# Performance work log

Hardware: AMD Instinct MI355X
Metric: run time of the kernel (lower is better)

The kernel has to match this reference:

```python
import jax, jax.numpy as jnp
import numpy as np
from jax import lax

N, P = 64, 7
C1, H1 = 256, 56
C2, H2 = 512, 28
C3, H3 = 1024, 14
HID1, HID2, HID3 = 256, 768, 1792
MLP1, MLP2, OUT = 3584, 1792, 512


def setup_inputs() -> dict:
    key = jax.random.key(0)
    ks = jax.random.split(key, 32)
    x1 = jax.random.normal(ks[0], (N, C1, H1, H1), jnp.float32)
    x2 = jax.random.normal(ks[1], (N, C2, H2, H2), jnp.float32)
    x3 = jax.random.normal(ks[2], (N, C3, H3, H3), jnp.float32)
    a = jax.random.randint(ks[3], (N, P, 2), 0, 56)
    b = jax.random.randint(ks[4], (N, P, 2), 0, 56)
    lo, hi = jnp.minimum(a, b), jnp.maximum(a, b)
    patchs = jnp.stack([lo[..., 0], hi[..., 0], lo[..., 1], hi[..., 1]], axis=-1)
    drop = jax.random.bernoulli(ks[5], 0.1, (N, P))
    patchs = jnp.where(drop[..., None], 0, patchs).astype(jnp.int32)

    def lin(k, o, i):
        return jax.random.normal(k, (o, i), jnp.float32) * 0.02

    def vec(k, o):
        return jax.random.normal(k, (o,), jnp.float32) * 0.02

    inp = {
        'x1': x1, 'x2': x2, 'x3': x3, 'patchs': patchs,
        # LSTM weights, torch gate order (i,f,g,o); bias = b_ih + b_hh combined
        'l1_wih': lin(ks[6], 4 * HID1, 256),  'l1_whh': lin(ks[7], 4 * HID1, HID1),  'l1_b': vec(ks[8], 4 * HID1),
        'l2_wih': lin(ks[9], 4 * HID2, 768),  'l2_whh': lin(ks[10], 4 * HID2, HID2), 'l2_b': vec(ks[11], 4 * HID2),
        'l3_wih': lin(ks[12], 4 * HID3, 1792),'l3_whh': lin(ks[13], 4 * HID3, HID3), 'l3_b': vec(ks[14], 4 * HID3),
        'aw1': lin(ks[15], MLP1, P * HID3), 'ab1': vec(ks[16], MLP1),
        'aw2': lin(ks[17], MLP2, MLP1),     'ab2': vec(ks[18], MLP2),
        'aw3': lin(ks[19], P, MLP2),        'ab3': vec(ks[20], P),
        'fw':  lin(ks[21], OUT, HID3),      'fb':  vec(ks[22], OUT),
    }
    return inp


def _crop_avg(x, patchs, num, den):
    """Batched data-dependent crop + avg-pool via 2D integral image.
    x: [N,C,H,W]; patchs: [N,P,4] ints (y0,y1,x0,x1) at 56-scale. Returns [N,P,C]."""
    y0 = (patchs[..., 0] * num) // den
    y1 = (patchs[..., 1] * num) // den
    x0 = (patchs[..., 2] * num) // den
    x1 = (patchs[..., 3] * num) // den
    S = jnp.cumsum(jnp.cumsum(x, axis=2), axis=3)
    S = jnp.pad(S, ((0, 0), (0, 0), (1, 0), (1, 0)))  # [N,C,H+1,W+1]
    bidx = jnp.arange(x.shape[0])[:, None]

    def g(Y, X):
        return S[bidx, :, Y, X]  # advanced idx split by ':' -> [N,P,C]

    tot = g(y1 + 1, x1 + 1) - g(y0, x1 + 1) - g(y1 + 1, x0) + g(y0, x0)
    area = ((y1 - y0 + 1) * (x1 - x0 + 1)).astype(x.dtype)[..., None]
    avg = tot / area
    zero = jnp.all(patchs == 0, axis=-1)  # all-zero box -> zero feature
    return jnp.where(zero[..., None], jnp.zeros((), x.dtype), avg)


def _lstm(x, wih, whh, b):
    """Single-layer batch-first LSTM, torch gate order i,f,g,o. x: [N,T,D] -> [N,T,H]."""
    Nb, T, _ = x.shape
    H = whh.shape[1]
    xg = jnp.einsum('ntd,gd->ntg', x, wih) + b  # precompute input gates

    def step(carry, xt):
        h, c = carry
        gates = xt + h @ whh.T
        i, f, g, o = jnp.split(gates, 4, axis=-1)
        c = jax.nn.sigmoid(f) * c + jax.nn.sigmoid(i) * jnp.tanh(g)
        h = jax.nn.sigmoid(o) * jnp.tanh(c)
        return (h, c), h

    h0 = jnp.zeros((Nb, H), x.dtype)
    _, hs = lax.scan(step, (h0, h0), jnp.swapaxes(xg, 0, 1))
    return jnp.swapaxes(hs, 0, 1)


def reference(x1, x2, x3, patchs,
              l1_wih, l1_whh, l1_b, l2_wih, l2_whh, l2_b, l3_wih, l3_whh, l3_b,
              aw1, ab1, aw2, ab2, aw3, ab3, fw, fb):
    local1 = _crop_avg(x1, patchs, 55, 55)                     # [N,7,256]
    rnn1 = _lstm(local1, l1_wih, l1_whh, l1_b)                 # [N,7,256]
    local2 = jnp.concatenate([_crop_avg(x2, patchs, 27, 55), rnn1], axis=2)   # [N,7,768]
    rnn2 = _lstm(local2, l2_wih, l2_whh, l2_b)                 # [N,7,768]
    local3 = jnp.concatenate([_crop_avg(x3, patchs, 13, 55), rnn2], axis=2)   # [N,7,1792]
    rnn3 = _lstm(local3, l3_wih, l3_whh, l3_b)                 # [N,7,1792]
    # attention pooling (dropout = identity in eval)
    flat = rnn3.reshape(rnn3.shape[0], -1)                     # [N,7*1792]
    h = jax.nn.relu(flat @ aw1.T + ab1)
    h = jax.nn.relu(h @ aw2.T + ab2)
    attn = jax.nn.relu(h @ aw3.T + ab3)                        # [N,7]
    alpha = jax.nn.softmax(attn, axis=1)
    feat = jnp.sum(rnn3 * alpha[:, :, None], axis=1)           # [N,1792]
    return feat @ fw.T + fb                                    # [N,512]
```

## Files before the change

kernel.cpp:

```cpp
#include <hip/hip_runtime.h>
#include <hip/hip_bf16.h>
#include <math.h>

#define NB 64
#define PP 7

typedef __attribute__((ext_vector_type(8))) short short8;
typedef __attribute__((ext_vector_type(4))) float f32x4;

static __device__ inline unsigned bf16r(float f) {
    unsigned u = __builtin_bit_cast(unsigned, f);
    u += 0x7fffu + ((u >> 16) & 1u);
    return u >> 16;
}
static __device__ inline unsigned pack2(float a, float b) {
    return bf16r(a) | (bf16r(b) << 16);
}

template<int H, int VEC, int GRP>
__device__ inline void crop_dev(
    int bx, int n, const float* __restrict__ x, const int* __restrict__ patchs,
    float* __restrict__ out, int C, int num, int den, int ldo, int col0)
{
    constexpr int USED = H / VEC;
    constexpr int PPWAVE = 64 / GRP;
    int tid = threadIdx.x, lane = tid & 63, wv = tid >> 6;
    int sub = lane / GRP, xl = lane & (GRP - 1);
    bool act = xl < USED;
    int c = bx * (4 * PPWAVE) + wv * PPWAVE + sub;

    int y0m1[PP], y1s[PP], x0s[PP], x1s[PP], zer[PP];
    float rarea[PP];
    #pragma unroll
    for (int p = 0; p < PP; ++p) {
        int p0 = patchs[(n * PP + p) * 4 + 0];
        int p1 = patchs[(n * PP + p) * 4 + 1];
        int p2 = patchs[(n * PP + p) * 4 + 2];
        int p3 = patchs[(n * PP + p) * 4 + 3];
        int y0 = p0 * num / den, y1 = p1 * num / den;
        int xx0 = p2 * num / den, xx1 = p3 * num / den;
        y0m1[p] = y0 - 1; y1s[p] = y1; x0s[p] = xx0; x1s[p] = xx1;
        rarea[p] = 1.f / (float)((y1 - y0 + 1) * (xx1 - xx0 + 1));
        zer[p] = (p0 | p1 | p2 | p3) == 0;
    }

    const float* pl = x + ((size_t)n * C + c) * (H * H) + (act ? xl * VEC : 0);

    float cc[VEC];
    float lo[PP][VEC], hi[PP][VEC];
    #pragma unroll
    for (int e = 0; e < VEC; ++e) cc[e] = 0.f;
    #pragma unroll
    for (int p = 0; p < PP; ++p)
        #pragma unroll
        for (int e = 0; e < VEC; ++e) { lo[p][e] = 0.f; hi[p][e] = 0.f; }

    #pragma unroll 4
    for (int y = 0; y < H; ++y) {
        float v[VEC];
        if constexpr (VEC == 4) {
            float4 t = *reinterpret_cast<const float4*>(pl + y * H);
            v[0] = t.x; v[1] = t.y; v[2] = t.z; v[3] = t.w;
        } else {
            float2 t = *reinterpret_cast<const float2*>(pl + y * H);
            v[0] = t.x; v[1] = t.y;
        }
        #pragma unroll
        for (int e = 0; e < VEC; ++e) cc[e] += v[e];
        #pragma unroll
        for (int p = 0; p < PP; ++p) {
            #pragma unroll
            for (int e = 0; e < VEC; ++e) {
                lo[p][e] = (y == y0m1[p]) ? cc[e] : lo[p][e];
                hi[p][e] = (y == y1s[p]) ? cc[e] : hi[p][e];
            }
        }
    }

    #pragma unroll
    for (int p = 0; p < PP; ++p) {
        float d = 0.f;
        #pragma unroll
        for (int e = 0; e < VEC; ++e) {
            int col = xl * VEC + e;
            if (col >= x0s[p] && col <= x1s[p]) d += hi[p][e] - lo[p][e];
        }
        #pragma unroll
        for (int off = GRP / 2; off >= 1; off >>= 1)
            d += __shfl_xor(d, off, 64);
        if (act && xl == 0)
            out[(size_t)(n * PP + p) * ldo + col0 + c] = zer[p] ? 0.f : d * rarea[p];
    }
}

__device__ inline void cvt_dev(
    int b, const float* __restrict__ in, uint4* __restrict__ out, int n8)
{
    int idx = b * 256 + threadIdx.x;
    if (idx >= n8) return;
    const float4* p = reinterpret_cast<const float4*>(in) + 2 * (size_t)idx;
    float4 a = p[0], bb = p[1];
    uint4 v;
    v.x = pack2(a.x, a.y); v.y = pack2(a.z, a.w);
    v.z = pack2(bb.x, bb.y); v.w = pack2(bb.z, bb.w);
    out[idx] = v;
}

__global__ __launch_bounds__(256) void prep_kernel(
    const float* __restrict__ x1, const float* __restrict__ x2,
    const float* __restrict__ x3, const int* __restrict__ patchs,
    float* __restrict__ local1, float* __restrict__ local2,
    float* __restrict__ local3,
    const float* __restrict__ l1_whh, uint4* __restrict__ whh1b,
    const float* __restrict__ l2_whh, uint4* __restrict__ whh2b,
    const float* __restrict__ l3_whh, uint4* __restrict__ whh3b,
    const float* __restrict__ l3_wih, uint4* __restrict__ wih3b)
{
    int b = blockIdx.x;
    if (b < 1024) {
        crop_dev<56, 4, 16>(b & 15, b >> 4, x1, patchs, local1, 256, 55, 55, 256, 0);
    } else if (b < 2048) {
        int bb = b - 1024;
        crop_dev<28, 4, 8>(bb & 15, bb >> 4, x2, patchs, local2, 512, 27, 55, 768, 0);
    } else if (b < 4096) {
        int bb = b - 2048;
        crop_dev<14, 2, 8>(bb & 31, bb >> 5, x3, patchs, local3, 1024, 13, 55, 1792, 0);
    } else if (b < 4224) {
        cvt_dev(b - 4096, l1_whh, whh1b, 32768);
    } else if (b < 5376) {
        cvt_dev(b - 4224, l2_whh, whh2b, 294912);
    } else if (b < 11648) {
        cvt_dev(b - 5376, l3_whh, whh3b, 1605632);
    } else {
        cvt_dev(b - 11648, l3_wih, wih3b, 1605632);
    }
}

template<int BN, bool WBF>
__global__ __launch_bounds__(256) void gemm_kernel(
    const float* __restrict__ X, int ldx,
    const void* __restrict__ Wp, int K,
    const float* __restrict__ bias,
    float* __restrict__ out, int ldo,
    int kchunk, int partial)
{
    constexpr int NF = BN / 64;
    __shared__ short Xs[64][72];
    __shared__ short Ws[BN][72];
    int tid = threadIdx.x;
    int lane = tid & 63, wv = tid >> 6;
    int m0 = blockIdx.y * 64;
    int o0 = blockIdx.x * BN;
    int z = blockIdx.z;
    int kbeg = z * kchunk, kend = kbeg + kchunk;

    f32x4 acc[4][NF];
    #pragma unroll
    for (int i = 0; i < 4; ++i)
        #pragma unroll
        for (int j = 0; j < NF; ++j)
            acc[i][j] = (f32x4){0.f, 0.f, 0.f, 0.f};

    for (int kb = kbeg; kb < kend; kb += 64) {
        #pragma unroll
        for (int i = 0; i < 2; ++i) {
            int cch = tid + 256 * i;
            int r = cch >> 3, col = (cch & 7) * 8;
            const float* src = X + (size_t)(m0 + r) * ldx + kb + col;
            float4 a = *reinterpret_cast<const float4*>(src);
            float4 b = *reinterpret_cast<const float4*>(src + 4);
            uint4 v;
            v.x = pack2(a.x, a.y); v.y = pack2(a.z, a.w);
            v.z = pack2(b.x, b.y); v.w = pack2(b.z, b.w);
            *reinterpret_cast<uint4*>(&Xs[r][col]) = v;
        }
        #pragma unroll
        for (int i = 0; i < 2 * NF; ++i) {
            int cch = tid + 256 * i;
            int r = cch >> 3, col = (cch & 7) * 8;
            if constexpr (WBF) {
                const short* srcw = (const short*)Wp + (size_t)(o0 + r) * K + kb + col;
                *reinterpret_cast<uint4*>(&Ws[r][col]) =
                    *reinterpret_cast<const uint4*>(srcw);
            } else {
                const float* srcw = (const float*)Wp + (size_t)(o0 + r) * K + kb + col;
                float4 c = *reinterpret_cast<const float4*>(srcw);
                float4 d = *reinterpret_cast<const float4*>(srcw + 4);
                uint4 w;
                w.x = pack2(c.x, c.y); w.y = pack2(c.z, c.w);
                w.z = pack2(d.x, d.y); w.w = pack2(d.z, d.w);
                *reinterpret_cast<uint4*>(&Ws[r][col]) = w;
            }
        }
        __syncthreads();
        #pragma unroll
        for (int kk = 0; kk < 64; kk += 32) {
            int ro = lane & 15, kof = kk + (lane >> 4) * 8;
            short8 b[NF];
            #pragma unroll
            for (int j = 0; j < NF; ++j)
                b[j] = *reinterpret_cast<const short8*>(
                    &Ws[wv * (BN / 4) + 16 * j + ro][kof]);
            #pragma unroll
            for (int i = 0; i < 4; ++i) {
                short8 a = *reinterpret_cast<const short8*>(&Xs[16 * i + ro][kof]);
                #pragma unroll
                for (int j = 0; j < NF; ++j)
                    acc[i][j] = __builtin_amdgcn_mfma_f32_16x16x32_bf16(
                        a, b[j], acc[i][j], 0, 0, 0);
            }
        }
        __syncthreads();
    }

    float* dst = out;
    if (partial) dst += (size_t)z * (gridDim.y * 64) * ldo;
    int mr = (lane >> 4) * 4;
    #pragma unroll
    for (int j = 0; j < NF; ++j) {
        int o = o0 + wv * (BN / 4) + 16 * j + (lane & 15);
        float bv = (!partial && bias) ? bias[o] : 0.f;
        #pragma unroll
        for (int i = 0; i < 4; ++i) {
            #pragma unroll
            for (int r = 0; r < 4; ++r) {
                int m = m0 + 16 * i + mr + r;
                dst[(size_t)m * ldo + o] = acc[i][j][r] + bv;
            }
        }
    }
}

__global__ __launch_bounds__(256) void reduce_kernel(
    const float* __restrict__ partial, int S, int M, int O,
    const float* __restrict__ bias, int relu, float* __restrict__ out)
{
    int idx = blockIdx.x * 256 + threadIdx.x;
    int tot = M * O;
    if (idx >= tot) return;
    float v = bias[idx % O];
    for (int s = 0; s < S; ++s) v += partial[(size_t)s * tot + idx];
    if (relu) v = fmaxf(v, 0.f);
    out[idx] = v;
}

__global__ __launch_bounds__(256) void lstm_cell_kernel(
    const float* __restrict__ partial, int S,
    const float* __restrict__ xgt, int ldxg,
    float* __restrict__ h, float* __restrict__ c,
    float* __restrict__ dest, int Hd, int ldd, int first)
{
    int idx = blockIdx.x * 256 + threadIdx.x;
    int q = Hd >> 2;
    if (idx >= NB * q) return;
    int n = idx / q, j4 = (idx - n * q) * 4;
    int H4 = 4 * Hd;

    f32x4 g[4];
    #pragma unroll
    for (int gi = 0; gi < 4; ++gi)
        g[gi] = *reinterpret_cast<const f32x4*>(xgt + (size_t)n * ldxg + gi * Hd + j4);
    if (!first) {
        for (int s = 0; s < S; ++s) {
            const float* pr = partial + ((size_t)s * NB + n) * H4;
            #pragma unroll
            for (int gi = 0; gi < 4; ++gi)
                g[gi] += *reinterpret_cast<const f32x4*>(pr + gi * Hd + j4);
        }
    }
    f32x4 cp = (f32x4){0.f, 0.f, 0.f, 0.f};
    if (!first) cp = *reinterpret_cast<const f32x4*>(c + (size_t)n * Hd + j4);

    f32x4 cn, hn;
    #pragma unroll
    for (int k = 0; k < 4; ++k) {
        float si = 1.f / (1.f + expf(-g[0][k]));
        float sf = 1.f / (1.f + expf(-g[1][k]));
        float so = 1.f / (1.f + expf(-g[3][k]));
        float cc = sf * cp[k] + si * tanhf(g[2][k]);
        cn[k] = cc;
        hn[k] = so * tanhf(cc);
    }
    *reinterpret_cast<f32x4*>(c + (size_t)n * Hd + j4) = cn;
    *reinterpret_cast<f32x4*>(h + (size_t)n * Hd + j4) = hn;
    *reinterpret_cast<f32x4*>(dest + (size_t)n * ldd + j4) = hn;
}

__global__ __launch_bounds__(256) void attn_fused_kernel(
    const float* __restrict__ h2, const float* __restrict__ aw3,
    const float* __restrict__ ab3, const float* __restrict__ rnn3,
    float* __restrict__ feat)
{
    int n = blockIdx.x;
    int tid = threadIdx.x, lane = tid & 63, wv = tid >> 6;
    __shared__ float logit[PP];
    __shared__ float alpha[PP];
    for (int p = wv; p < PP; p += 4) {
        float s = 0.f;
        for (int k = lane; k < 1792; k += 64)
            s += h2[n * 1792 + k] * aw3[p * 1792 + k];
        #pragma unroll
        for (int off = 32; off; off >>= 1) s += __shfl_down(s, off, 64);
        if (lane == 0) logit[p] = fmaxf(s + ab3[p], 0.f);
    }
    __syncthreads();
    if (tid == 0) {
        float a[PP], mx = -1e30f;
        for (int p = 0; p < PP; ++p) { a[p] = logit[p]; mx = fmaxf(mx, a[p]); }
        float s = 0.f;
        for (int p = 0; p < PP; ++p) { a[p] = expf(a[p] - mx); s += a[p]; }
        for (int p = 0; p < PP; ++p) alpha[p] = a[p] / s;
    }
    __syncthreads();
    for (int j = tid; j < 1792; j += 256) {
        float s = 0.f;
        #pragma unroll
        for (int p = 0; p < PP; ++p)
            s += rnn3[((size_t)n * PP + p) * 1792 + j] * alpha[p];
        feat[(size_t)n * 1792 + j] = s;
    }
}


extern "C" void kernel_launch(void* const* d_in, const int* in_sizes, int n_in,
                              void* d_out, int out_size, void* d_ws, size_t ws_size,
                              hipStream_t stream) {
    const float* x1 = (const float*)d_in[0];
    const float* x2 = (const float*)d_in[1];
    const float* x3 = (const float*)d_in[2];
    const int* patchs = (const int*)d_in[3];
    const float* l1_wih = (const float*)d_in[4];
    const float* l1_whh = (const float*)d_in[5];
    const float* l1_b   = (const float*)d_in[6];
    const float* l2_wih = (const float*)d_in[7];
    const float* l2_whh = (const float*)d_in[8];
    const float* l2_b   = (const float*)d_in[9];
    const float* l3_wih = (const float*)d_in[10];
    const float* l3_whh = (const float*)d_in[11];
    const float* l3_b   = (const float*)d_in[12];
    const float* aw1 = (const float*)d_in[13];
    const float* ab1 = (const float*)d_in[14];
    const float* aw2 = (const float*)d_in[15];
    const float* ab2 = (const float*)d_in[16];
    const float* aw3 = (const float*)d_in[17];
    const float* ab3 = (const float*)d_in[18];
    const float* fw  = (const float*)d_in[19];
    const float* fb  = (const float*)d_in[20];
    float* out = (float*)d_out;

    float* ws = (float*)d_ws;
    float* local1 = ws;
    float* local2 = ws + 114688;
    float* local3 = ws + 458752;
    float* rnn3   = local3;
    float* xg     = ws + 1261568;
    float* partial= ws + 4472832;
    float* hbuf   = ws + 10895360;
    float* cbuf   = ws + 11010048;
    float* h1     = ws + 11124736;
    float* h2     = ws + 11354112;
    float* feat   = ws + 11468800;
    float* wb     = ws + 11583488;
    short* whh1b  = (short*)wb;
    short* whh2b  = (short*)(wb + 131072);
    short* whh3b  = (short*)(wb + 131072 + 1179648);
    short* wih3b  = (short*)(wb + 131072 + 1179648 + 6422528);

    prep_kernel<<<17920, 256, 0, stream>>>(
        x1, x2, x3, patchs, local1, local2, local3,
        l1_whh, (uint4*)whh1b, l2_whh, (uint4*)whh2b, l3_whh, (uint4*)whh3b,
        l3_wih, (uint4*)wih3b);

    {
        int H = 256, H4 = 1024;
        gemm_kernel<64, false><<<dim3(16, 7, 1), 256, 0, stream>>>(
            local1, 256, l1_wih, 256, l1_b, xg, H4, 256, 0);
        for (int t = 0; t < PP; ++t) {
            if (t > 0)
                gemm_kernel<64, true><<<dim3(16, 1, 4), 256, 0, stream>>>(
                    hbuf, H, whh1b, H, nullptr, partial, H4, 64, 1);
            lstm_cell_kernel<<<(NB * H / 4 + 255) / 256, 256, 0, stream>>>(
                partial, 4, xg + (size_t)t * H4, PP * H4,
                hbuf, cbuf, local2 + (size_t)t * 768 + 512, H, PP * 768, t == 0);
        }
    }
    {
        int H = 768, H4 = 3072;
        gemm_kernel<64, false><<<dim3(48, 7, 1), 256, 0, stream>>>(
            local2, 768, l2_wih, 768, l2_b, xg, H4, 768, 0);
        for (int t = 0; t < PP; ++t) {
            if (t > 0)
                gemm_kernel<64, true><<<dim3(48, 1, 12), 256, 0, stream>>>(
                    hbuf, H, whh2b, H, nullptr, partial, H4, 64, 1);
            lstm_cell_kernel<<<(NB * H / 4 + 255) / 256, 256, 0, stream>>>(
                partial, 12, xg + (size_t)t * H4, PP * H4,
                hbuf, cbuf, local3 + (size_t)t * 1792 + 1024, H, PP * 1792, t == 0);
        }
    }
    {
        int H = 1792, H4 = 7168;
        gemm_kernel<128, true><<<dim3(56, 7, 1), 256, 0, stream>>>(
            local3, 1792, wih3b, 1792, l3_b, xg, H4, 1792, 0);
        for (int t = 0; t < PP; ++t) {
            if (t > 0)
                gemm_kernel<128, true><<<dim3(56, 1, 14), 256, 0, stream>>>(
                    hbuf, H, whh3b, H, nullptr, partial, H4, 128, 1);
            lstm_cell_kernel<<<(NB * H / 4 + 255) / 256, 256, 0, stream>>>(
                partial, 14, xg + (size_t)t * H4, PP * H4,
                hbuf, cbuf, rnn3 + (size_t)t * 1792, H, PP * 1792, t == 0);
        }
    }

    gemm_kernel<64, false><<<dim3(56, 1, 14), 256, 0, stream>>>(
        rnn3, 12544, aw1, 12544, nullptr, partial, 3584, 896, 1);
    reduce_kernel<<<(64 * 3584 + 255) / 256, 256, 0, stream>>>(
        partial, 14, 64, 3584, ab1, 1, h1);
    gemm_kernel<64, false><<<dim3(28, 1, 7), 256, 0, stream>>>(
        h1, 3584, aw2, 3584, nullptr, partial, 1792, 512, 1);
    reduce_kernel<<<(64 * 1792 + 255) / 256, 256, 0, stream>>>(
        partial, 7, 64, 1792, ab2, 1, h2);
    attn_fused_kernel<<<NB, 256, 0, stream>>>(h2, aw3, ab3, rnn3, feat);
    gemm_kernel<64, false><<<dim3(8, 1, 7), 256, 0, stream>>>(
        feat, 1792, fw, 1792, nullptr, partial, 512, 256, 1);
    reduce_kernel<<<(64 * 512 + 255) / 256, 256, 0, stream>>>(
        partial, 7, 64, 512, fb, 0, out);
}
```

Measured before the change: 617.0 us.

## Run LSTM layers 1-2 as persistent kernels with grid-wide atomic barriers

Layers 1 and 2 now run as one persistent kernel each. Every block owns 16 hidden units across all four gates, computes the recurrent matmul with MFMA, keeps the cell state in registers, and syncs timesteps through atomic counters in ping-pong h buffers. This replaces about 13 small GEMM and cell launches per layer, along with their split-K partial round trips. Layer 3 drops the bf16 conversion of l3_wih and reads fp32 weights in its input GEMM, and its recurrent split-K is cut from 14 to 7 slices. The risks are spin-barrier correctness, which needs all blocks co-resident, and lower parallelism when only 16 or 48 blocks are active.

```diff
diff --git a/kernel.cpp b/kernel.cpp
--- a/kernel.cpp
+++ b/kernel.cpp
@@ -114,7 +114,7 @@
     const float* __restrict__ l1_whh, uint4* __restrict__ whh1b,
     const float* __restrict__ l2_whh, uint4* __restrict__ whh2b,
     const float* __restrict__ l3_whh, uint4* __restrict__ whh3b,
-    const float* __restrict__ l3_wih, uint4* __restrict__ wih3b)
+    int* __restrict__ cnt)
 {
     int b = blockIdx.x;
     if (b < 1024) {
@@ -132,7 +132,7 @@
     } else if (b < 11648) {
         cvt_dev(b - 5376, l3_whh, whh3b, 1605632);
     } else {
-        cvt_dev(b - 11648, l3_wih, wih3b, 1605632);
+        if (threadIdx.x < 16) cnt[threadIdx.x] = 0;
     }
 }
 
@@ -227,6 +227,109 @@
                 int m = m0 + 16 * i + mr + r;
                 dst[(size_t)m * ldo + o] = acc[i][j][r] + bv;
             }
+        }
+    }
+}
+
+__global__ __launch_bounds__(256) void lstm_persist_kernel(
+    const short* __restrict__ whhb, int H,
+    const float* __restrict__ xg,
+    float* __restrict__ destb, int destHT, int col0,
+    float* __restrict__ hA, float* __restrict__ hB,
+    int* __restrict__ cnt, int nblk)
+{
+    __shared__ short Hs[64][72];
+    __shared__ short Ws[64][72];
+    __shared__ float gbuf[4][64][20];
+    int tid = threadIdx.x, lane = tid & 63, wv = tid >> 6;
+    int jt = blockIdx.x, j0 = jt * 16;
+    int H4 = 4 * H, ldxg = PP * H4;
+    int n = tid >> 2, u4 = (tid & 3) * 4;
+    f32x4 creg = (f32x4){0.f, 0.f, 0.f, 0.f};
+
+    for (int t = 0; t < PP; ++t) {
+        f32x4 g[4];
+        #pragma unroll
+        for (int gate = 0; gate < 4; ++gate)
+            g[gate] = *reinterpret_cast<const f32x4*>(
+                xg + (size_t)t * H4 + (size_t)n * ldxg + gate * H + j0 + u4);
+
+        if (t > 0) {
+            const float* hp = (t & 1) ? hA : hB;
+            f32x4 acc[4];
+            #pragma unroll
+            for (int i = 0; i < 4; ++i) acc[i] = (f32x4){0.f, 0.f, 0.f, 0.f};
+            for (int kb = 0; kb < H; kb += 64) {
+                #pragma unroll
+                for (int i = 0; i < 2; ++i) {
+                    int cch = tid + 256 * i;
+                    int r = cch >> 3, col = (cch & 7) * 8;
+                    const float* src = hp + (size_t)r * H + kb + col;
+                    float4 a = *reinterpret_cast<const float4*>(src);
+                    float4 b = *reinterpret_cast<const float4*>(src + 4);
+                    uint4 v;
+                    v.x = pack2(a.x, a.y); v.y = pack2(a.z, a.w);
+                    v.z = pack2(b.x, b.y); v.w = pack2(b.z, b.w);
+                    *reinterpret_cast<uint4*>(&Hs[r][col]) = v;
+                    int wr = (r >> 4) * H + j0 + (r & 15);
+                    const short* srcw = whhb + (size_t)wr * H + kb + col;
+                    *reinterpret_cast<uint4*>(&Ws[r][col]) =
+                        *reinterpret_cast<const uint4*>(srcw);
+                }
+                __syncthreads();
+                #pragma unroll
+                for (int kk = 0; kk < 64; kk += 32) {
+                    int ro = lane & 15, kof = kk + (lane >> 4) * 8;
+                    short8 b = *reinterpret_cast<const short8*>(&Ws[wv * 16 + ro][kof]);
+                    #pragma unroll
+                    for (int i = 0; i < 4; ++i) {
+                        short8 a = *reinterpret_cast<const short8*>(&Hs[16 * i + ro][kof]);
+                        acc[i] = __builtin_amdgcn_mfma_f32_16x16x32_bf16(
+                            a, b, acc[i], 0, 0, 0);
+                    }
+                }
+                __syncthreads();
+            }
+            int mr = (lane >> 4) * 4, jj = lane & 15;
+            #pragma unroll
+            for (int i = 0; i < 4; ++i)
+                #pragma unroll
+                for (int r = 0; r < 4; ++r)
+                    gbuf[wv][16 * i + mr + r][jj] = acc[i][r];
+            __syncthreads();
+            #pragma unroll
+            for (int gate = 0; gate < 4; ++gate)
+                g[gate] += *reinterpret_cast<const f32x4*>(&gbuf[gate][n][u4]);
+        }
+
+        f32x4 cn, hn;
+        #pragma unroll
+        for (int k = 0; k < 4; ++k) {
+            float si = 1.f / (1.f + expf(-g[0][k]));
+            float sf = 1.f / (1.f + expf(-g[1][k]));
+            float so = 1.f / (1.f + expf(-g[3][k]));
+            float cc = sf * creg[k] + si * tanhf(g[2][k]);
+            cn[k] = cc;
+            hn[k] = so * tanhf(cc);
+        }
+        creg = cn;
+        float* hw = (t & 1) ? hB : hA;
+        *reinterpret_cast<f32x4*>(hw + (size_t)n * H + j0 + u4) = hn;
+        *reinterpret_cast<f32x4*>(
+            destb + (size_t)t * destHT + (size_t)n * (PP * destHT) + col0 + j0 + u4) = hn;
+
+        if (t < PP - 1) {
+            __threadfence();
+            __syncthreads();
+            if (tid == 0) {
+                __hip_atomic_fetch_add(cnt + t, 1, __ATOMIC_ACQ_REL,
+                                       __HIP_MEMORY_SCOPE_AGENT);
+                while (__hip_atomic_load(cnt + t, __ATOMIC_ACQUIRE,
+                                         __HIP_MEMORY_SCOPE_AGENT) < nblk)
+                    __builtin_amdgcn_s_sleep(1);
+            }
+            __syncthreads();
+            __threadfence();
         }
     }
 }
@@ -355,59 +458,48 @@
     float* rnn3   = local3;
     float* xg     = ws + 1261568;
     float* partial= ws + 4472832;
-    float* hbuf   = ws + 10895360;
-    float* cbuf   = ws + 11010048;
-    float* h1     = ws + 11124736;
-    float* h2     = ws + 11354112;
-    float* feat   = ws + 11468800;
-    float* wb     = ws + 11583488;
+    float* hbufA  = ws + 7684096;
+    float* hbufB  = ws + 7798784;
+    float* cbuf   = ws + 7913472;
+    float* h1     = ws + 8028160;
+    float* h2     = ws + 8257536;
+    float* feat   = ws + 8372224;
+    float* wb     = ws + 8486912;
     short* whh1b  = (short*)wb;
     short* whh2b  = (short*)(wb + 131072);
     short* whh3b  = (short*)(wb + 131072 + 1179648);
-    short* wih3b  = (short*)(wb + 131072 + 1179648 + 6422528);
-
-    prep_kernel<<<17920, 256, 0, stream>>>(
+    int*   cnt    = (int*)(wb + 131072 + 1179648 + 6422528);
+
+    prep_kernel<<<11649, 256, 0, stream>>>(
         x1, x2, x3, patchs, local1, local2, local3,
         l1_whh, (uint4*)whh1b, l2_whh, (uint4*)whh2b, l3_whh, (uint4*)whh3b,
-        l3_wih, (uint4*)wih3b);
+        cnt);
 
     {
         int H = 256, H4 = 1024;
         gemm_kernel<64, false><<<dim3(16, 7, 1), 256, 0, stream>>>(
             local1, 256, l1_wih, 256, l1_b, xg, H4, 256, 0);
-        for (int t = 0; t < PP; ++t) {
-            if (t > 0)
-                gemm_kernel<64, true><<<dim3(16, 1, 4), 256, 0, stream>>>(
-                    hbuf, H, whh1b, H, nullptr, partial, H4, 64, 1);
-            lstm_cell_kernel<<<(NB * H / 4 + 255) / 256, 256, 0, stream>>>(
-                partial, 4, xg + (size_t)t * H4, PP * H4,
-                hbuf, cbuf, local2 + (size_t)t * 768 + 512, H, PP * 768, t == 0);
-        }
+        lstm_persist_kernel<<<16, 256, 0, stream>>>(
+            whh1b, H, xg, local2, 768, 512, hbufA, hbufB, cnt, 16);
     }
     {
         int H = 768, H4 = 3072;
         gemm_kernel<64, false><<<dim3(48, 7, 1), 256, 0, stream>>>(
             local2, 768, l2_wih, 768, l2_b, xg, H4, 768, 0);
+        lstm_persist_kernel<<<48, 256, 0, stream>>>(
+            whh2b, H, xg, local3, 1792, 1024, hbufA, hbufB, cnt + 8, 48);
+    }
+    {
+        int H = 1792, H4 = 7168;
+        gemm_kernel<128, false><<<dim3(56, 7, 1), 256, 0, stream>>>(
+            local3, 1792, l3_wih, 1792, l3_b, xg, H4, 1792, 0);
         for (int t = 0; t < PP; ++t) {
             if (t > 0)
-                gemm_kernel<64, true><<<dim3(48, 1, 12), 256, 0, stream>>>(
-                    hbuf, H, whh2b, H, nullptr, partial, H4, 64, 1);
+                gemm_kernel<128, true><<<dim3(56, 1, 7), 256, 0, stream>>>(
+                    hbufA, H, whh3b, H, nullptr, partial, H4, 256, 1);
             lstm_cell_kernel<<<(NB * H / 4 + 255) / 256, 256, 0, stream>>>(
-                partial, 12, xg + (size_t)t * H4, PP * H4,
-                hbuf, cbuf, local3 + (size_t)t * 1792 + 1024, H, PP * 1792, t == 0);
-        }
-    }
-    {
-        int H = 1792, H4 = 7168;
-        gemm_kernel<128, true><<<dim3(56, 7, 1), 256, 0, stream>>>(
-            local3, 1792, wih3b, 1792, l3_b, xg, H4, 1792, 0);
-        for (int t = 0; t < PP; ++t) {
-            if (t > 0)
-                gemm_kernel<128, true><<<dim3(56, 1, 14), 256, 0, stream>>>(
-                    hbuf, H, whh3b, H, nullptr, partial, H4, 128, 1);
-            lstm_cell_kernel<<<(NB * H / 4 + 255) / 256, 256, 0, stream>>>(
-                partial, 14, xg + (size_t)t * H4, PP * H4,
-                hbuf, cbuf, rnn3 + (size_t)t * 1792, H, PP * 1792, t == 0);
+                partial, 7, xg + (size_t)t * H4, PP * H4,
+                hbufA, cbuf, rnn3 + (size_t)t * 1792, H, PP * 1792, t == 0);
         }
     }
 
```

Result: slower. 660.5 us (+7.0%).
